# Kernel optimization log

Measured on AMD Instinct MI355X. Metric: run time of the kernel, lower is better.

The kernel has to match this reference:

```python
import jax, jax.numpy as jnp
import numpy as np


def _gcn_conv(x, edge_index, W, b):
    # PyG GCNConv: h = x @ W; out = D^{-1/2}(A+I)D^{-1/2} h + b
    N = x.shape[0]
    src, dst = edge_index[0], edge_index[1]
    # degree with self-loops (edge weights = 1)
    deg = jax.ops.segment_sum(jnp.ones(src.shape[0], x.dtype), dst, num_segments=N) + 1.0
    dis = jax.lax.rsqrt(deg)  # deg >= 1 so finite
    h = x @ W  # [N, F_out]
    norm = dis[src] * dis[dst]  # [E]
    msg = h[src] * norm[:, None]  # [E, F_out] -- dominant memory traffic
    agg = jax.ops.segment_sum(msg, dst, num_segments=N)
    # self-loop contribution: norm_ii = dis_i^2
    out = agg + h * (dis * dis)[:, None] + b
    return out


def setup_inputs() -> dict:
    key = jax.random.key(0)
    k1, k2, k3, k4, k5, k6 = jax.random.split(key, 6)
    N, E = 100000, 1600000
    in_ch, hid, out_ch = 256, 128, 64  # hid = 2*out_channels
    x = jax.random.normal(k1, (N, in_ch), dtype=jnp.float32)
    edge_index = jax.random.randint(k2, (2, E), 0, N, dtype=jnp.int64)
    # Glorot-style init for GCN weights, zero bias (PyG default)
    W1 = jax.random.normal(k3, (in_ch, hid), dtype=jnp.float32) / np.sqrt(in_ch)
    b1 = jnp.zeros((hid,), jnp.float32)
    W2 = jax.random.normal(k4, (hid, out_ch), dtype=jnp.float32) / np.sqrt(hid)
    b2 = jnp.zeros((out_ch,), jnp.float32)
    return {"x": x, "edge_index": edge_index, "W1": W1, "b1": b1, "W2": W2, "b2": b2}


def reference(x, edge_index, W1, b1, W2, b2):
    # Encoder.forward: k=2 layers of activation(GCNConv(x, edge_index))
    h = jax.nn.relu(_gcn_conv(x, edge_index, W1, b1))
    h = jax.nn.relu(_gcn_conv(h, edge_index, W2, b2))
    return h
```

## Files before the change

### kernel.cpp

```cpp
#include <hip/hip_runtime.h>
#include <math.h>

#define THREADS 256

static inline int cdiv(long long a, long long b) { return (int)((a + b - 1) / b); }

typedef __attribute__((ext_vector_type(8))) short bf16x8;
typedef __attribute__((ext_vector_type(4))) float f32x4;

__device__ inline unsigned f2bf_rne_u(float f) {
    unsigned u = __builtin_bit_cast(unsigned, f);
    return (u + 0x7FFFu + ((u >> 16) & 1u)) >> 16;
}
__device__ inline float bfu2f(unsigned h) {
    unsigned u = h << 16;
    return __builtin_bit_cast(float, u);
}


__device__ __forceinline__ void hist_body8(const int* __restrict__ dst, int* __restrict__ deg,
                                           int* __restrict__ rank, int E, int blk) {
    int base = (blk * THREADS + (int)threadIdx.x) * 8;
    if (base + 7 < E) {
        int4 d0 = *(const int4*)(dst + base);
        int4 d1 = *(const int4*)(dst + base + 4);
        int4 r0, r1;
        r0.x = atomicAdd(&deg[d0.x], 1);
        r0.y = atomicAdd(&deg[d0.y], 1);
        r0.z = atomicAdd(&deg[d0.z], 1);
        r0.w = atomicAdd(&deg[d0.w], 1);
        r1.x = atomicAdd(&deg[d1.x], 1);
        r1.y = atomicAdd(&deg[d1.y], 1);
        r1.z = atomicAdd(&deg[d1.z], 1);
        r1.w = atomicAdd(&deg[d1.w], 1);
        *(int4*)(rank + base) = r0;
        *(int4*)(rank + base + 4) = r1;
    } else {
        for (int e = base; e < E; ++e) rank[e] = atomicAdd(&deg[dst[e]], 1);
    }
}

__device__ __forceinline__ void bfrag_unit(const float* __restrict__ W, short* __restrict__ frag,
                                           int NCT, int ctks, int lane) {
    int Nn = NCT * 16;
    int ct = ctks % NCT;
    int ks = ctks / NCT;
    int colc = ct * 16 + (lane & 15);
    int kbase = ks * 32 + (lane >> 4) * 8;
    short* base = frag + (size_t)ctks * 1024 + lane * 8;
    #pragma unroll
    for (int j = 0; j < 8; ++j) {
        float v = W[(size_t)(kbase + j) * Nn + colc];
        unsigned h = f2bf_rne_u(v);
        base[j] = (short)h;
        base[512 + j] = (short)f2bf_rne_u(v - bfu2f(h));
    }
}

__device__ __forceinline__ void fill_body(const int* __restrict__ src, const int* __restrict__ dst,
                                          const int* __restrict__ rank, const int* __restrict__ rowptr,
                                          int* __restrict__ col, int E, int blk) {
    int base = (blk * THREADS + (int)threadIdx.x) * 4;
    if (base + 3 < E) {
        int4 d = *(const int4*)(dst + base);
        int4 r = *(const int4*)(rank + base);
        int4 s = *(const int4*)(src + base);
        col[rowptr[d.x] + r.x] = s.x;
        col[rowptr[d.y] + r.y] = s.y;
        col[rowptr[d.z] + r.z] = s.z;
        col[rowptr[d.w] + r.w] = s.w;
    } else {
        for (int e = base; e < E; ++e)
            col[rowptr[dst[e]] + rank[e]] = src[e];
    }
}

template<int NCT, int KS>
__device__ __forceinline__ void gemm_body(const float* __restrict__ A, const short* __restrict__ Bfrag,
                                          unsigned short* __restrict__ H, int M, int blk) {
    constexpr int K = KS * 32;
    constexpr int Nn = NCT * 16;
    const int lane = threadIdx.x & 63;
    const int wave = threadIdx.x >> 6;
    const int rowBase = blk * 128 + wave * 32;
    const int arow0 = rowBase + (lane & 15);
    const int kgrp = (lane >> 4) * 8;

    f32x4 acc[2][NCT] = {};

    for (int ks = 0; ks < KS; ++ks) {
        const int kbase = ks * 32 + kgrp;
        bf16x8 ahi[2], alo[2];
        #pragma unroll
        for (int t = 0; t < 2; ++t) {
            int r = arow0 + t * 16;
            if (r >= M) r = M - 1;
            const float* ap = A + (size_t)r * K + kbase;
            float4 v0 = *(const float4*)ap;
            float4 v1 = *(const float4*)(ap + 4);
            float av[8] = {v0.x, v0.y, v0.z, v0.w, v1.x, v1.y, v1.z, v1.w};
            #pragma unroll
            for (int j = 0; j < 8; ++j) {
                unsigned h = f2bf_rne_u(av[j]);
                ahi[t][j] = (short)h;
                alo[t][j] = (short)f2bf_rne_u(av[j] - bfu2f(h));
            }
        }
        #pragma unroll
        for (int ct = 0; ct < NCT; ++ct) {
            const short* bp = Bfrag + (size_t)(ks * NCT + ct) * 1024 + lane * 8;
            bf16x8 bhi = *(const bf16x8*)bp;
            bf16x8 blo = *(const bf16x8*)(bp + 512);
            #pragma unroll
            for (int t = 0; t < 2; ++t) {
                acc[t][ct] = __builtin_amdgcn_mfma_f32_16x16x32_bf16(ahi[t], bhi, acc[t][ct], 0, 0, 0);
                acc[t][ct] = __builtin_amdgcn_mfma_f32_16x16x32_bf16(ahi[t], blo, acc[t][ct], 0, 0, 0);
                acc[t][ct] = __builtin_amdgcn_mfma_f32_16x16x32_bf16(alo[t], bhi, acc[t][ct], 0, 0, 0);
            }
        }
    }

    const int drow0 = rowBase + (lane >> 4) * 4;
    #pragma unroll
    for (int t = 0; t < 2; ++t) {
        #pragma unroll
        for (int r = 0; r < 4; ++r) {
            int row = drow0 + t * 16 + r;
            if (row < M) {
                unsigned short* hp = H + (size_t)row * Nn + (lane & 15);
                #pragma unroll
                for (int ct = 0; ct < NCT; ++ct)
                    hp[ct * 16] = (unsigned short)f2bf_rne_u(acc[t][ct][r]);
            }
        }
    }
}


__global__ __launch_bounds__(THREADS)
void zero_bfrag_kernel(int* __restrict__ deg, int N,
                       const float* __restrict__ W1, short* __restrict__ bf1,
                       const float* __restrict__ W2, short* __restrict__ bf2, int nbZero) {
    int b = (int)blockIdx.x;
    if (b < nbZero) {
        int base = (b * THREADS + (int)threadIdx.x) * 4;
        if (base + 3 < N) {
            *(int4*)(deg + base) = make_int4(0, 0, 0, 0);
        } else {
            for (int i = base; i < N; ++i) deg[i] = 0;
        }
    } else {
        int u = (b - nbZero) * 4 + ((int)threadIdx.x >> 6);
        int lane = threadIdx.x & 63;
        if (u < 64) bfrag_unit(W1, bf1, 8, u, lane);
        else if (u < 80) bfrag_unit(W2, bf2, 4, u - 64, lane);
    }
}

__global__ __launch_bounds__(THREADS)
void hist_gemm1_kernel(const int* __restrict__ dst, int* __restrict__ deg,
                       int* __restrict__ rank, int E,
                       const float* __restrict__ A, const short* __restrict__ Bfrag,
                       unsigned short* __restrict__ H, int M,
                       int nbHist, int nbGemm) {
    int b = (int)blockIdx.x;
    int total = nbHist + nbGemm;
    long long t = (long long)b * nbGemm;
    int gBefore = (int)(t / total);
    bool isG = (((long long)(b + 1) * nbGemm) / total) > gBefore;
    if (isG) gemm_body<8, 8>(A, Bfrag, H, M, gBefore);
    else     hist_body8(dst, deg, rank, E, b - gBefore);
}

__global__ __launch_bounds__(THREADS)
void fill_col_rank_kernel(const int* __restrict__ src, const int* __restrict__ dst,
                          const int* __restrict__ rank, const int* __restrict__ rowptr,
                          int* __restrict__ col, int E) {
    fill_body(src, dst, rank, rowptr, col, E, (int)blockIdx.x);
}

template<int NCT, int KS>
__global__ __launch_bounds__(THREADS)
void mfma_gemm_bf16out_kernel(const float* __restrict__ A, const short* __restrict__ Bfrag,
                              unsigned short* __restrict__ H, int M) {
    gemm_body<NCT, KS>(A, Bfrag, H, M, (int)blockIdx.x);
}


#define SCAN_BLOCK 256
#define SCAN_ITEMS 4

__global__ __launch_bounds__(SCAN_BLOCK)
void scan_block_kernel(const int* __restrict__ in, int* __restrict__ out,
                       int* __restrict__ blockSums, float* __restrict__ dis, int n) {
    __shared__ int sdata[SCAN_BLOCK];
    int base = blockIdx.x * (SCAN_BLOCK * SCAN_ITEMS);
    int tid = threadIdx.x;
    int v[SCAN_ITEMS];
    int sum = 0;
    #pragma unroll
    for (int k = 0; k < SCAN_ITEMS; ++k) {
        int idx = base + tid * SCAN_ITEMS + k;
        v[k] = (idx < n) ? in[idx] : 0;
        if (idx < n) dis[idx] = rsqrtf((float)v[k] + 1.0f);
        sum += v[k];
    }
    sdata[tid] = sum;
    __syncthreads();
    for (int off = 1; off < SCAN_BLOCK; off <<= 1) {
        int t = (tid >= off) ? sdata[tid - off] : 0;
        __syncthreads();
        sdata[tid] += t;
        __syncthreads();
    }
    if (tid == SCAN_BLOCK - 1) blockSums[blockIdx.x] = sdata[SCAN_BLOCK - 1];
    int run = (tid == 0) ? 0 : sdata[tid - 1];
    #pragma unroll
    for (int k = 0; k < SCAN_ITEMS; ++k) {
        int idx = base + tid * SCAN_ITEMS + k;
        if (idx < n) out[idx] = run;
        run += v[k];
    }
}

__global__ __launch_bounds__(SCAN_BLOCK)
void scan_sums_kernel(int* __restrict__ blockSums, int nB) {
    __shared__ int sdata[SCAN_BLOCK];
    int tid = threadIdx.x;
    sdata[tid] = (tid < nB) ? blockSums[tid] : 0;
    __syncthreads();
    for (int off = 1; off < SCAN_BLOCK; off <<= 1) {
        int t = (tid >= off) ? sdata[tid - off] : 0;
        __syncthreads();
        sdata[tid] += t;
        __syncthreads();
    }
    int excl = (tid == 0) ? 0 : sdata[tid - 1];
    if (tid < nB) blockSums[tid] = excl;
}

__global__ __launch_bounds__(SCAN_BLOCK)
void scan_add_kernel(int* __restrict__ out, const int* __restrict__ blockSums,
                     int n, int E) {
    int base = blockIdx.x * (SCAN_BLOCK * SCAN_ITEMS);
    int add = blockSums[blockIdx.x];
    #pragma unroll
    for (int k = 0; k < SCAN_ITEMS; ++k) {
        int idx = base + threadIdx.x * SCAN_ITEMS + k;
        if (idx < n) out[idx] += add;
    }
    if (blockIdx.x == 0 && threadIdx.x == 0) out[n] = E;
}


template<int F, int VEC>
__global__ __launch_bounds__(THREADS)
void gather_bf16_kernel(const unsigned short* __restrict__ g, const int* __restrict__ col,
                        const int* __restrict__ rowptr, const float* __restrict__ dis,
                        const float* __restrict__ bias, float* __restrict__ out, int N) {
    int wid = (int)((blockIdx.x * (long long)blockDim.x + threadIdx.x) >> 6);
    wid = __builtin_amdgcn_readfirstlane(wid);
    const int lane = threadIdx.x & 63;
    if (wid >= N) return;
    const float di = dis[wid];
    const int loff = lane * VEC;

    float acc0 = 0.0f, acc1 = 0.0f;

    auto loadrow = [&](int s) -> unsigned {
        const unsigned short* p = g + (size_t)s * F + loff;
        if (VEC == 2) return *(const unsigned*)p;
        else return (unsigned)*p;
    };
    auto addconv = [&](unsigned u, float w) {
        if (VEC == 2) {
            acc0 += w * bfu2f(u & 0xFFFFu);
            acc1 += w * __builtin_bit_cast(float, u & 0xFFFF0000u);
        } else {
            acc0 += w * bfu2f(u);
        }
    };

    addconv(loadrow(wid), di);

    int start = __builtin_amdgcn_readfirstlane(rowptr[wid]);
    int end   = __builtin_amdgcn_readfirstlane(rowptr[wid + 1]);
    const int* c = col + start;
    int rem = end - start;

    if (rem >= 4) {
        int s0 = __builtin_amdgcn_readfirstlane(c[0]);
        int s1 = __builtin_amdgcn_readfirstlane(c[1]);
        int s2 = __builtin_amdgcn_readfirstlane(c[2]);
        int s3 = __builtin_amdgcn_readfirstlane(c[3]);
        float w0 = dis[s0], w1 = dis[s1], w2 = dis[s2], w3 = dis[s3];
        unsigned u0 = loadrow(s0), u1 = loadrow(s1), u2 = loadrow(s2), u3 = loadrow(s3);
        c += 4; rem -= 4;
        while (rem >= 4) {
            int t0 = __builtin_amdgcn_readfirstlane(c[0]);
            int t1 = __builtin_amdgcn_readfirstlane(c[1]);
            int t2 = __builtin_amdgcn_readfirstlane(c[2]);
            int t3 = __builtin_amdgcn_readfirstlane(c[3]);
            float x0 = dis[t0], x1 = dis[t1], x2 = dis[t2], x3 = dis[t3];
            unsigned v0 = loadrow(t0), v1 = loadrow(t1), v2 = loadrow(t2), v3 = loadrow(t3);
            addconv(u0, w0); addconv(u1, w1); addconv(u2, w2); addconv(u3, w3);
            u0 = v0; u1 = v1; u2 = v2; u3 = v3;
            w0 = x0; w1 = x1; w2 = x2; w3 = x3;
            c += 4; rem -= 4;
        }
        addconv(u0, w0); addconv(u1, w1); addconv(u2, w2); addconv(u3, w3);
    }
    while (rem > 0) {
        int s = __builtin_amdgcn_readfirstlane(c[0]);
        addconv(loadrow(s), dis[s]);
        ++c; --rem;
    }

    float* orow = out + (size_t)wid * F + loff;
    float v0 = di * acc0 + bias[loff];
    if (VEC == 2) {
        float v1 = di * acc1 + bias[loff + 1];
        float2 st = make_float2(fmaxf(v0, 0.0f), fmaxf(v1, 0.0f));
        *(float2*)orow = st;
    } else {
        *orow = fmaxf(v0, 0.0f);
    }
}


#define BM 64
#define BN 64
#define BK 16

__global__ __launch_bounds__(THREADS)
void sgemm_kernel(const float* __restrict__ A, const float* __restrict__ B,
                  float* __restrict__ C, int M, int N, int K) {
    __shared__ float As[BK][BM + 1];
    __shared__ float Bs[BK][BN + 1];

    const int tid = threadIdx.x;
    const int tr = tid / 16;
    const int tc = tid % 16;
    const int rowBase = blockIdx.y * BM;
    const int colBase = blockIdx.x * BN;

    float acc[4][4] = {};

    for (int k0 = 0; k0 < K; k0 += BK) {
        #pragma unroll
        for (int i = tid; i < BM * BK; i += THREADS) {
            int r = i / BK, c = i % BK;
            int gr = rowBase + r;
            As[c][r] = (gr < M) ? A[(size_t)gr * K + k0 + c] : 0.0f;
        }
        #pragma unroll
        for (int i = tid; i < BK * BN; i += THREADS) {
            int r = i / BN, c = i % BN;
            Bs[r][c] = B[(size_t)(k0 + r) * N + colBase + c];
        }
        __syncthreads();

        #pragma unroll
        for (int k = 0; k < BK; ++k) {
            float a[4], b[4];
            #pragma unroll
            for (int m = 0; m < 4; ++m) a[m] = As[k][tr * 4 + m];
            #pragma unroll
            for (int n = 0; n < 4; ++n) b[n] = Bs[k][tc * 4 + n];
            #pragma unroll
            for (int m = 0; m < 4; ++m)
                #pragma unroll
                for (int n = 0; n < 4; ++n)
                    acc[m][n] += a[m] * b[n];
        }
        __syncthreads();
    }

    #pragma unroll
    for (int m = 0; m < 4; ++m) {
        int gr = rowBase + tr * 4 + m;
        if (gr >= M) continue;
        #pragma unroll
        for (int n = 0; n < 4; ++n) {
            C[(size_t)gr * N + colBase + tc * 4 + n] = acc[m][n];
        }
    }
}

__global__ __launch_bounds__(THREADS)
void init_agg_kernel(const float* __restrict__ h, const float* __restrict__ dis,
                     float* __restrict__ agg, int N, int F) {
    int i = blockIdx.x * blockDim.x + threadIdx.x;
    int total = N * (F / 4);
    if (i >= total) return;
    int node = i / (F / 4);
    float d = dis[node];
    float w = d * d;
    float4 v = ((const float4*)h)[i];
    v.x *= w; v.y *= w; v.z *= w; v.w *= w;
    ((float4*)agg)[i] = v;
}

__global__ __launch_bounds__(THREADS)
void edge_scatter_kernel(const float* __restrict__ h, const int* __restrict__ src,
                         const int* __restrict__ dst, const float* __restrict__ dis,
                         float* __restrict__ agg, int E, int F) {
    int lanesPerEdge = F / 4;
    int tid = blockIdx.x * blockDim.x + threadIdx.x;
    int e = tid / lanesPerEdge;
    int c = tid % lanesPerEdge;
    if (e >= E) return;
    int s = src[e];
    int d = dst[e];
    float w = dis[s] * dis[d];
    float4 hv = ((const float4*)(h + (size_t)s * F))[c];
    float* ap = agg + (size_t)d * F + (size_t)c * 4;
    atomicAdd(ap + 0, hv.x * w);
    atomicAdd(ap + 1, hv.y * w);
    atomicAdd(ap + 2, hv.z * w);
    atomicAdd(ap + 3, hv.w * w);
}

__global__ __launch_bounds__(THREADS)
void finalize_kernel(const float* __restrict__ agg, const float* __restrict__ b,
                     float* __restrict__ out, int N, int F) {
    int i = blockIdx.x * blockDim.x + threadIdx.x;
    int total = N * (F / 4);
    if (i >= total) return;
    int c4 = i % (F / 4);
    float4 bv = ((const float4*)b)[c4];
    float4 v = ((const float4*)agg)[i];
    v.x = fmaxf(v.x + bv.x, 0.0f);
    v.y = fmaxf(v.y + bv.y, 0.0f);
    v.z = fmaxf(v.z + bv.z, 0.0f);
    v.w = fmaxf(v.w + bv.w, 0.0f);
    ((float4*)out)[i] = v;
}

__global__ __launch_bounds__(THREADS)
void fdeg_kernel(const int* __restrict__ dst, float* __restrict__ deg, int E) {
    int i = blockIdx.x * blockDim.x + threadIdx.x;
    if (i < E) atomicAdd(&deg[dst[i]], 1.0f);
}

__global__ __launch_bounds__(THREADS)
void fdis_kernel(float* __restrict__ deg, int N) {
    int i = blockIdx.x * blockDim.x + threadIdx.x;
    if (i < N) deg[i] = rsqrtf(deg[i] + 1.0f);
}


extern "C" void kernel_launch(void* const* d_in, const int* in_sizes, int n_in,
                              void* d_out, int out_size, void* d_ws, size_t ws_size,
                              hipStream_t stream) {
    const float* x  = (const float*)d_in[0];
    const int*   ei = (const int*)d_in[1];
    const float* W1 = (const float*)d_in[2];
    const float* b1 = (const float*)d_in[3];
    const float* W2 = (const float*)d_in[4];
    const float* b2 = (const float*)d_in[5];

    const int E    = in_sizes[1] / 2;
    const int hid  = in_sizes[3];
    const int outc = in_sizes[5];
    const int inc  = in_sizes[2] / hid;
    const int N    = in_sizes[0] / inc;

    const int* src = ei;
    const int* dst = ei + E;
    float* out = (float*)d_out;
    char* ws = (char*)d_ws;

    auto al = [](size_t v) { return (v + 255) & ~(size_t)255; };
    size_t o_dis  = 0;
    size_t o_deg  = al(o_dis + (size_t)N * 4);
    size_t o_rp   = al(o_deg + (size_t)N * 4);
    size_t o_bs   = al(o_rp + ((size_t)N + 1) * 4);
    size_t o_col  = al(o_bs + 4096);
    size_t o_rank = al(o_col + (size_t)E * 4);
    size_t o_bf1  = al(o_rank + (size_t)E * 4);
    size_t o_bf2  = al(o_bf1 + 131072);
    size_t o_G    = al(o_bf2 + 32768);
    size_t o_B    = al(o_G + (size_t)N * hid * 2);
    size_t need   = o_B + (size_t)N * hid * 4;

    if (ws_size >= need && N <= SCAN_BLOCK * SCAN_BLOCK * SCAN_ITEMS &&
        hid == 128 && outc == 64 && inc == 256) {
        float* dis    = (float*)(ws + o_dis);
        int*   deg    = (int*)(ws + o_deg);
        int*   rowptr = (int*)(ws + o_rp);
        int*   bsums  = (int*)(ws + o_bs);
        int*   col    = (int*)(ws + o_col);
        int*   rank   = (int*)(ws + o_rank);
        short* bf1    = (short*)(ws + o_bf1);
        short* bf2    = (short*)(ws + o_bf2);
        unsigned short* gbuf = (unsigned short*)(ws + o_G);
        float* out1   = (float*)(ws + o_B);

        const int nbZero  = cdiv(N, 4 * THREADS);
        const int nbHist  = cdiv(E, 8 * THREADS);
        const int nbGemm1 = cdiv(N, 128);
        const int nbFill  = cdiv(E, 4 * THREADS);

        zero_bfrag_kernel<<<nbZero + 20, THREADS, 0, stream>>>(deg, N, W1, bf1, W2, bf2, nbZero);

        hist_gemm1_kernel<<<nbHist + nbGemm1, THREADS, 0, stream>>>(
            dst, deg, rank, E, x, bf1, gbuf, N, nbHist, nbGemm1);

        int nB = cdiv(N, SCAN_BLOCK * SCAN_ITEMS);
        scan_block_kernel<<<nB, SCAN_BLOCK, 0, stream>>>(deg, rowptr, bsums, dis, N);
        scan_sums_kernel<<<1, SCAN_BLOCK, 0, stream>>>(bsums, nB);
        scan_add_kernel<<<nB, SCAN_BLOCK, 0, stream>>>(rowptr, bsums, N, E);

        fill_col_rank_kernel<<<nbFill, THREADS, 0, stream>>>(src, dst, rank, rowptr, col, E);

        gather_bf16_kernel<128, 2><<<cdiv((long long)N * 64, THREADS), THREADS, 0, stream>>>(
            gbuf, col, rowptr, dis, b1, out1, N);

        mfma_gemm_bf16out_kernel<4, 4><<<cdiv(N, 128), THREADS, 0, stream>>>(out1, bf2, gbuf, N);
        gather_bf16_kernel<64, 1><<<cdiv((long long)N * 64, THREADS), THREADS, 0, stream>>>(
            gbuf, col, rowptr, dis, b2, out, N);
        return;
    }

    float* dis = (float*)ws;
    size_t off1 = ((size_t)N * 4 + 255) & ~(size_t)255;
    float* h1 = (float*)(ws + off1);
    size_t off2 = off1 + ((((size_t)N * hid * 4) + 255) & ~(size_t)255);
    float* agg1 = (float*)(ws + off2);
    float* h2   = agg1;
    float* agg2 = agg1 + (size_t)N * outc;

    hipMemsetAsync(dis, 0, (size_t)N * 4, stream);
    fdeg_kernel<<<cdiv(E, THREADS), THREADS, 0, stream>>>(dst, dis, E);
    fdis_kernel<<<cdiv(N, THREADS), THREADS, 0, stream>>>(dis, N);

    {
        dim3 grid(hid / BN, cdiv(N, BM));
        sgemm_kernel<<<grid, THREADS, 0, stream>>>(x, W1, h1, N, hid, inc);
    }
    init_agg_kernel<<<cdiv((long long)N * hid / 4, THREADS), THREADS, 0, stream>>>(h1, dis, agg1, N, hid);
    edge_scatter_kernel<<<cdiv((long long)E * (hid / 4), THREADS), THREADS, 0, stream>>>(
        h1, src, dst, dis, agg1, E, hid);
    finalize_kernel<<<cdiv((long long)N * hid / 4, THREADS), THREADS, 0, stream>>>(agg1, b1, h1, N, hid);

    {
        dim3 grid(outc / BN, cdiv(N, BM));
        sgemm_kernel<<<grid, THREADS, 0, stream>>>(h1, W2, h2, N, outc, hid);
    }
    init_agg_kernel<<<cdiv((long long)N * outc / 4, THREADS), THREADS, 0, stream>>>(h2, dis, agg2, N, outc);
    edge_scatter_kernel<<<cdiv((long long)E * (outc / 4), THREADS), THREADS, 0, stream>>>(
        h2, src, dst, dis, agg2, E, outc);
    finalize_kernel<<<cdiv((long long)N * outc / 4, THREADS), THREADS, 0, stream>>>(agg2, b2, out, N, outc);
}
```

Measured before the change: 260.1 us.

## Privatize degree histogram into eight copies and split hist from GEMM1

The degree histogram is spread across eight sub-histograms chosen by block index, which cuts atomic contention on each counter. The scan kernels now add up the eight counts and build per-copy row offsets (rp8), and the CSR fill uses these with the per-copy rank. The fused hist+GEMM1 launch is split into two separate kernels, and the GEMM body now prefetches the next K-slice of A into registers. This adds extra memory traffic for eight N-sized arrays and for the rp8 reads, plus one more kernel launch.

```diff
diff --git a/kernel.cpp b/kernel.cpp
--- a/kernel.cpp
+++ b/kernel.cpp
@@ -2,6 +2,8 @@
 #include <math.h>
 
 #define THREADS 256
+#define HIST_ILP 8
+#define EPB_SHIFT 11
 
 static inline int cdiv(long long a, long long b) { return (int)((a + b - 1) / b); }
 
@@ -18,10 +20,132 @@
 }
 
 
-__device__ __forceinline__ void hist_body8(const int* __restrict__ dst, int* __restrict__ deg,
-                                           int* __restrict__ rank, int E, int blk) {
-    int base = (blk * THREADS + (int)threadIdx.x) * 8;
-    if (base + 7 < E) {
+__device__ __forceinline__ void bfrag_unit(const float* __restrict__ W, short* __restrict__ frag,
+                                           int NCT, int ctks, int lane) {
+    int Nn = NCT * 16;
+    int ct = ctks % NCT;
+    int ks = ctks / NCT;
+    int colc = ct * 16 + (lane & 15);
+    int kbase = ks * 32 + (lane >> 4) * 8;
+    short* base = frag + (size_t)ctks * 1024 + lane * 8;
+    #pragma unroll
+    for (int j = 0; j < 8; ++j) {
+        float v = W[(size_t)(kbase + j) * Nn + colc];
+        unsigned h = f2bf_rne_u(v);
+        base[j] = (short)h;
+        base[512 + j] = (short)f2bf_rne_u(v - bfu2f(h));
+    }
+}
+
+template<int NCT, int KS>
+__device__ __forceinline__ void gemm_body(const float* __restrict__ A, const short* __restrict__ Bfrag,
+                                          unsigned short* __restrict__ H, int M, int blk) {
+    constexpr int K = KS * 32;
+    constexpr int Nn = NCT * 16;
+    const int lane = threadIdx.x & 63;
+    const int wave = threadIdx.x >> 6;
+    const int rowBase = blk * 128 + wave * 32;
+    const int kgrp = (lane >> 4) * 8;
+
+    const float* ap0;
+    const float* ap1;
+    {
+        int r0 = rowBase + (lane & 15);      if (r0 >= M) r0 = M - 1;
+        int r1 = rowBase + (lane & 15) + 16; if (r1 >= M) r1 = M - 1;
+        ap0 = A + (size_t)r0 * K + kgrp;
+        ap1 = A + (size_t)r1 * K + kgrp;
+    }
+
+    f32x4 acc[2][NCT] = {};
+
+    float4 c00 = *(const float4*)(ap0);
+    float4 c01 = *(const float4*)(ap0 + 4);
+    float4 c10 = *(const float4*)(ap1);
+    float4 c11 = *(const float4*)(ap1 + 4);
+
+    for (int ks = 0; ks < KS; ++ks) {
+        float4 n00, n01, n10, n11;
+        if (ks + 1 < KS) {
+            const float* p0 = ap0 + (size_t)(ks + 1) * 32;
+            const float* p1 = ap1 + (size_t)(ks + 1) * 32;
+            n00 = *(const float4*)(p0);
+            n01 = *(const float4*)(p0 + 4);
+            n10 = *(const float4*)(p1);
+            n11 = *(const float4*)(p1 + 4);
+        }
+        bf16x8 ahi[2], alo[2];
+        {
+            float av0[8] = {c00.x, c00.y, c00.z, c00.w, c01.x, c01.y, c01.z, c01.w};
+            float av1[8] = {c10.x, c10.y, c10.z, c10.w, c11.x, c11.y, c11.z, c11.w};
+            #pragma unroll
+            for (int j = 0; j < 8; ++j) {
+                unsigned h0 = f2bf_rne_u(av0[j]);
+                ahi[0][j] = (short)h0;
+                alo[0][j] = (short)f2bf_rne_u(av0[j] - bfu2f(h0));
+                unsigned h1 = f2bf_rne_u(av1[j]);
+                ahi[1][j] = (short)h1;
+                alo[1][j] = (short)f2bf_rne_u(av1[j] - bfu2f(h1));
+            }
+        }
+        #pragma unroll
+        for (int ct = 0; ct < NCT; ++ct) {
+            const short* bp = Bfrag + (size_t)(ks * NCT + ct) * 1024 + lane * 8;
+            bf16x8 bhi = *(const bf16x8*)bp;
+            bf16x8 blo = *(const bf16x8*)(bp + 512);
+            #pragma unroll
+            for (int t = 0; t < 2; ++t) {
+                acc[t][ct] = __builtin_amdgcn_mfma_f32_16x16x32_bf16(ahi[t], bhi, acc[t][ct], 0, 0, 0);
+                acc[t][ct] = __builtin_amdgcn_mfma_f32_16x16x32_bf16(ahi[t], blo, acc[t][ct], 0, 0, 0);
+                acc[t][ct] = __builtin_amdgcn_mfma_f32_16x16x32_bf16(alo[t], bhi, acc[t][ct], 0, 0, 0);
+            }
+        }
+        c00 = n00; c01 = n01; c10 = n10; c11 = n11;
+    }
+
+    const int drow0 = rowBase + (lane >> 4) * 4;
+    #pragma unroll
+    for (int t = 0; t < 2; ++t) {
+        #pragma unroll
+        for (int r = 0; r < 4; ++r) {
+            int row = drow0 + t * 16 + r;
+            if (row < M) {
+                unsigned short* hp = H + (size_t)row * Nn + (lane & 15);
+                #pragma unroll
+                for (int ct = 0; ct < NCT; ++ct)
+                    hp[ct * 16] = (unsigned short)f2bf_rne_u(acc[t][ct][r]);
+            }
+        }
+    }
+}
+
+
+__global__ __launch_bounds__(THREADS)
+void zero_bfrag_kernel(int* __restrict__ deg8, int total8,
+                       const float* __restrict__ W1, short* __restrict__ bf1,
+                       const float* __restrict__ W2, short* __restrict__ bf2, int nbZero) {
+    int b = (int)blockIdx.x;
+    if (b < nbZero) {
+        int base = (b * THREADS + (int)threadIdx.x) * 4;
+        if (base + 3 < total8) {
+            *(int4*)(deg8 + base) = make_int4(0, 0, 0, 0);
+        } else {
+            for (int i = base; i < total8; ++i) deg8[i] = 0;
+        }
+    } else {
+        int u = (b - nbZero) * 4 + ((int)threadIdx.x >> 6);
+        int lane = threadIdx.x & 63;
+        if (u < 64) bfrag_unit(W1, bf1, 8, u, lane);
+        else if (u < 80) bfrag_unit(W2, bf2, 4, u - 64, lane);
+    }
+}
+
+__global__ __launch_bounds__(THREADS)
+void hist8_kernel(const int* __restrict__ dst, int* __restrict__ deg8,
+                  int* __restrict__ rank, int E, int N) {
+    int b = (int)blockIdx.x;
+    int* deg = deg8 + (size_t)(b & 7) * N;
+    int base = (b << EPB_SHIFT) + (int)threadIdx.x * HIST_ILP;
+    if (base + HIST_ILP - 1 < E) {
         int4 d0 = *(const int4*)(dst + base);
         int4 d1 = *(const int4*)(dst + base + 4);
         int4 r0, r1;
@@ -40,158 +164,12 @@
     }
 }
 
-__device__ __forceinline__ void bfrag_unit(const float* __restrict__ W, short* __restrict__ frag,
-                                           int NCT, int ctks, int lane) {
-    int Nn = NCT * 16;
-    int ct = ctks % NCT;
-    int ks = ctks / NCT;
-    int colc = ct * 16 + (lane & 15);
-    int kbase = ks * 32 + (lane >> 4) * 8;
-    short* base = frag + (size_t)ctks * 1024 + lane * 8;
-    #pragma unroll
-    for (int j = 0; j < 8; ++j) {
-        float v = W[(size_t)(kbase + j) * Nn + colc];
-        unsigned h = f2bf_rne_u(v);
-        base[j] = (short)h;
-        base[512 + j] = (short)f2bf_rne_u(v - bfu2f(h));
-    }
-}
-
-__device__ __forceinline__ void fill_body(const int* __restrict__ src, const int* __restrict__ dst,
-                                          const int* __restrict__ rank, const int* __restrict__ rowptr,
-                                          int* __restrict__ col, int E, int blk) {
-    int base = (blk * THREADS + (int)threadIdx.x) * 4;
-    if (base + 3 < E) {
-        int4 d = *(const int4*)(dst + base);
-        int4 r = *(const int4*)(rank + base);
-        int4 s = *(const int4*)(src + base);
-        col[rowptr[d.x] + r.x] = s.x;
-        col[rowptr[d.y] + r.y] = s.y;
-        col[rowptr[d.z] + r.z] = s.z;
-        col[rowptr[d.w] + r.w] = s.w;
-    } else {
-        for (int e = base; e < E; ++e)
-            col[rowptr[dst[e]] + rank[e]] = src[e];
-    }
-}
-
-template<int NCT, int KS>
-__device__ __forceinline__ void gemm_body(const float* __restrict__ A, const short* __restrict__ Bfrag,
-                                          unsigned short* __restrict__ H, int M, int blk) {
-    constexpr int K = KS * 32;
-    constexpr int Nn = NCT * 16;
-    const int lane = threadIdx.x & 63;
-    const int wave = threadIdx.x >> 6;
-    const int rowBase = blk * 128 + wave * 32;
-    const int arow0 = rowBase + (lane & 15);
-    const int kgrp = (lane >> 4) * 8;
-
-    f32x4 acc[2][NCT] = {};
-
-    for (int ks = 0; ks < KS; ++ks) {
-        const int kbase = ks * 32 + kgrp;
-        bf16x8 ahi[2], alo[2];
-        #pragma unroll
-        for (int t = 0; t < 2; ++t) {
-            int r = arow0 + t * 16;
-            if (r >= M) r = M - 1;
-            const float* ap = A + (size_t)r * K + kbase;
-            float4 v0 = *(const float4*)ap;
-            float4 v1 = *(const float4*)(ap + 4);
-            float av[8] = {v0.x, v0.y, v0.z, v0.w, v1.x, v1.y, v1.z, v1.w};
-            #pragma unroll
-            for (int j = 0; j < 8; ++j) {
-                unsigned h = f2bf_rne_u(av[j]);
-                ahi[t][j] = (short)h;
-                alo[t][j] = (short)f2bf_rne_u(av[j] - bfu2f(h));
-            }
-        }
-        #pragma unroll
-        for (int ct = 0; ct < NCT; ++ct) {
-            const short* bp = Bfrag + (size_t)(ks * NCT + ct) * 1024 + lane * 8;
-            bf16x8 bhi = *(const bf16x8*)bp;
-            bf16x8 blo = *(const bf16x8*)(bp + 512);
-            #pragma unroll
-            for (int t = 0; t < 2; ++t) {
-                acc[t][ct] = __builtin_amdgcn_mfma_f32_16x16x32_bf16(ahi[t], bhi, acc[t][ct], 0, 0, 0);
-                acc[t][ct] = __builtin_amdgcn_mfma_f32_16x16x32_bf16(ahi[t], blo, acc[t][ct], 0, 0, 0);
-                acc[t][ct] = __builtin_amdgcn_mfma_f32_16x16x32_bf16(alo[t], bhi, acc[t][ct], 0, 0, 0);
-            }
-        }
-    }
-
-    const int drow0 = rowBase + (lane >> 4) * 4;
-    #pragma unroll
-    for (int t = 0; t < 2; ++t) {
-        #pragma unroll
-        for (int r = 0; r < 4; ++r) {
-            int row = drow0 + t * 16 + r;
-            if (row < M) {
-                unsigned short* hp = H + (size_t)row * Nn + (lane & 15);
-                #pragma unroll
-                for (int ct = 0; ct < NCT; ++ct)
-                    hp[ct * 16] = (unsigned short)f2bf_rne_u(acc[t][ct][r]);
-            }
-        }
-    }
-}
-
-
-__global__ __launch_bounds__(THREADS)
-void zero_bfrag_kernel(int* __restrict__ deg, int N,
-                       const float* __restrict__ W1, short* __restrict__ bf1,
-                       const float* __restrict__ W2, short* __restrict__ bf2, int nbZero) {
-    int b = (int)blockIdx.x;
-    if (b < nbZero) {
-        int base = (b * THREADS + (int)threadIdx.x) * 4;
-        if (base + 3 < N) {
-            *(int4*)(deg + base) = make_int4(0, 0, 0, 0);
-        } else {
-            for (int i = base; i < N; ++i) deg[i] = 0;
-        }
-    } else {
-        int u = (b - nbZero) * 4 + ((int)threadIdx.x >> 6);
-        int lane = threadIdx.x & 63;
-        if (u < 64) bfrag_unit(W1, bf1, 8, u, lane);
-        else if (u < 80) bfrag_unit(W2, bf2, 4, u - 64, lane);
-    }
-}
-
-__global__ __launch_bounds__(THREADS)
-void hist_gemm1_kernel(const int* __restrict__ dst, int* __restrict__ deg,
-                       int* __restrict__ rank, int E,
-                       const float* __restrict__ A, const short* __restrict__ Bfrag,
-                       unsigned short* __restrict__ H, int M,
-                       int nbHist, int nbGemm) {
-    int b = (int)blockIdx.x;
-    int total = nbHist + nbGemm;
-    long long t = (long long)b * nbGemm;
-    int gBefore = (int)(t / total);
-    bool isG = (((long long)(b + 1) * nbGemm) / total) > gBefore;
-    if (isG) gemm_body<8, 8>(A, Bfrag, H, M, gBefore);
-    else     hist_body8(dst, deg, rank, E, b - gBefore);
-}
-
-__global__ __launch_bounds__(THREADS)
-void fill_col_rank_kernel(const int* __restrict__ src, const int* __restrict__ dst,
-                          const int* __restrict__ rank, const int* __restrict__ rowptr,
-                          int* __restrict__ col, int E) {
-    fill_body(src, dst, rank, rowptr, col, E, (int)blockIdx.x);
-}
-
-template<int NCT, int KS>
-__global__ __launch_bounds__(THREADS)
-void mfma_gemm_bf16out_kernel(const float* __restrict__ A, const short* __restrict__ Bfrag,
-                              unsigned short* __restrict__ H, int M) {
-    gemm_body<NCT, KS>(A, Bfrag, H, M, (int)blockIdx.x);
-}
-
 
 #define SCAN_BLOCK 256
 #define SCAN_ITEMS 4
 
 __global__ __launch_bounds__(SCAN_BLOCK)
-void scan_block_kernel(const int* __restrict__ in, int* __restrict__ out,
+void scan_block_kernel(const int* __restrict__ deg8, int* __restrict__ out,
                        int* __restrict__ blockSums, float* __restrict__ dis, int n) {
     __shared__ int sdata[SCAN_BLOCK];
     int base = blockIdx.x * (SCAN_BLOCK * SCAN_ITEMS);
@@ -201,9 +179,14 @@
     #pragma unroll
     for (int k = 0; k < SCAN_ITEMS; ++k) {
         int idx = base + tid * SCAN_ITEMS + k;
-        v[k] = (idx < n) ? in[idx] : 0;
-        if (idx < n) dis[idx] = rsqrtf((float)v[k] + 1.0f);
-        sum += v[k];
+        int s8 = 0;
+        if (idx < n) {
+            #pragma unroll
+            for (int c = 0; c < 8; ++c) s8 += deg8[(size_t)c * n + idx];
+            dis[idx] = rsqrtf((float)s8 + 1.0f);
+        }
+        v[k] = s8;
+        sum += s8;
     }
     sdata[tid] = sum;
     __syncthreads();
@@ -240,16 +223,56 @@
 }
 
 __global__ __launch_bounds__(SCAN_BLOCK)
-void scan_add_kernel(int* __restrict__ out, const int* __restrict__ blockSums,
-                     int n, int E) {
+void scan_add_rp8_kernel(int* __restrict__ rowptr, const int* __restrict__ blockSums,
+                         const int* __restrict__ deg8, int* __restrict__ rp8,
+                         int n, int E) {
     int base = blockIdx.x * (SCAN_BLOCK * SCAN_ITEMS);
     int add = blockSums[blockIdx.x];
     #pragma unroll
     for (int k = 0; k < SCAN_ITEMS; ++k) {
         int idx = base + threadIdx.x * SCAN_ITEMS + k;
-        if (idx < n) out[idx] += add;
-    }
-    if (blockIdx.x == 0 && threadIdx.x == 0) out[n] = E;
+        if (idx < n) {
+            int val = rowptr[idx] + add;
+            rowptr[idx] = val;
+            int run = val;
+            #pragma unroll
+            for (int c = 0; c < 8; ++c) {
+                rp8[(size_t)c * n + idx] = run;
+                run += deg8[(size_t)c * n + idx];
+            }
+        }
+    }
+    if (blockIdx.x == 0 && threadIdx.x == 0) rowptr[n] = E;
+}
+
+__global__ __launch_bounds__(THREADS)
+void fill_col_rp8_kernel(const int* __restrict__ src, const int* __restrict__ dst,
+                         const int* __restrict__ rank, const int* __restrict__ rp8,
+                         int* __restrict__ col, int E, int N) {
+    int base = ((int)blockIdx.x * THREADS + (int)threadIdx.x) * 4;
+    if (base + 3 < E) {
+        int c = (base >> EPB_SHIFT) & 7;
+        const int* rp = rp8 + (size_t)c * N;
+        int4 d = *(const int4*)(dst + base);
+        int4 r = *(const int4*)(rank + base);
+        int4 s = *(const int4*)(src + base);
+        col[rp[d.x] + r.x] = s.x;
+        col[rp[d.y] + r.y] = s.y;
+        col[rp[d.z] + r.z] = s.z;
+        col[rp[d.w] + r.w] = s.w;
+    } else {
+        for (int e = base; e < E; ++e) {
+            int c = (e >> EPB_SHIFT) & 7;
+            col[rp8[(size_t)c * N + dst[e]] + rank[e]] = src[e];
+        }
+    }
+}
+
+template<int NCT, int KS>
+__global__ __launch_bounds__(THREADS)
+void mfma_gemm_bf16out_kernel(const float* __restrict__ A, const short* __restrict__ Bfrag,
+                              unsigned short* __restrict__ H, int M) {
+    gemm_body<NCT, KS>(A, Bfrag, H, M, (int)blockIdx.x);
 }
 
 
@@ -473,9 +496,10 @@
 
     auto al = [](size_t v) { return (v + 255) & ~(size_t)255; };
     size_t o_dis  = 0;
-    size_t o_deg  = al(o_dis + (size_t)N * 4);
-    size_t o_rp   = al(o_deg + (size_t)N * 4);
-    size_t o_bs   = al(o_rp + ((size_t)N + 1) * 4);
+    size_t o_deg8 = al(o_dis + (size_t)N * 4);
+    size_t o_rp   = al(o_deg8 + (size_t)N * 32);
+    size_t o_rp8  = al(o_rp + ((size_t)N + 1) * 4);
+    size_t o_bs   = al(o_rp8 + (size_t)N * 32);
     size_t o_col  = al(o_bs + 4096);
     size_t o_rank = al(o_col + (size_t)E * 4);
     size_t o_bf1  = al(o_rank + (size_t)E * 4);
@@ -487,8 +511,9 @@
     if (ws_size >= need && N <= SCAN_BLOCK * SCAN_BLOCK * SCAN_ITEMS &&
         hid == 128 && outc == 64 && inc == 256) {
         float* dis    = (float*)(ws + o_dis);
-        int*   deg    = (int*)(ws + o_deg);
+        int*   deg8   = (int*)(ws + o_deg8);
         int*   rowptr = (int*)(ws + o_rp);
+        int*   rp8    = (int*)(ws + o_rp8);
         int*   bsums  = (int*)(ws + o_bs);
         int*   col    = (int*)(ws + o_col);
         int*   rank   = (int*)(ws + o_rank);
@@ -497,22 +522,23 @@
         unsigned short* gbuf = (unsigned short*)(ws + o_G);
         float* out1   = (float*)(ws + o_B);
 
-        const int nbZero  = cdiv(N, 4 * THREADS);
-        const int nbHist  = cdiv(E, 8 * THREADS);
+        const int nbZero  = cdiv((long long)N * 8, 4 * THREADS);
+        const int nbHist  = cdiv(E, THREADS * HIST_ILP);
         const int nbGemm1 = cdiv(N, 128);
         const int nbFill  = cdiv(E, 4 * THREADS);
 
-        zero_bfrag_kernel<<<nbZero + 20, THREADS, 0, stream>>>(deg, N, W1, bf1, W2, bf2, nbZero);
-
-        hist_gemm1_kernel<<<nbHist + nbGemm1, THREADS, 0, stream>>>(
-            dst, deg, rank, E, x, bf1, gbuf, N, nbHist, nbGemm1);
+        zero_bfrag_kernel<<<nbZero + 20, THREADS, 0, stream>>>(deg8, N * 8, W1, bf1, W2, bf2, nbZero);
+
+        hist8_kernel<<<nbHist, THREADS, 0, stream>>>(dst, deg8, rank, E, N);
+
+        mfma_gemm_bf16out_kernel<8, 8><<<nbGemm1, THREADS, 0, stream>>>(x, bf1, gbuf, N);
 
         int nB = cdiv(N, SCAN_BLOCK * SCAN_ITEMS);
-        scan_block_kernel<<<nB, SCAN_BLOCK, 0, stream>>>(deg, rowptr, bsums, dis, N);
+        scan_block_kernel<<<nB, SCAN_BLOCK, 0, stream>>>(deg8, rowptr, bsums, dis, N);
         scan_sums_kernel<<<1, SCAN_BLOCK, 0, stream>>>(bsums, nB);
-        scan_add_kernel<<<nB, SCAN_BLOCK, 0, stream>>>(rowptr, bsums, N, E);
-
-        fill_col_rank_kernel<<<nbFill, THREADS, 0, stream>>>(src, dst, rank, rowptr, col, E);
+        scan_add_rp8_kernel<<<nB, SCAN_BLOCK, 0, stream>>>(rowptr, bsums, deg8, rp8, N, E);
+
+        fill_col_rp8_kernel<<<nbFill, THREADS, 0, stream>>>(src, dst, rank, rp8, col, E, N);
 
         gather_bf16_kernel<128, 2><<<cdiv((long long)N * 64, THREADS), THREADS, 0, stream>>>(
             gbuf, col, rowptr, dis, b1, out1, N);
```

Measured after the change: 292.6 us. 1.13x slower.
